# Kernel optimization log

Measured on AMD Instinct MI355X. Metric: run time of the kernel, lower is better.

## Reference

```python
import jax, jax.numpy as jnp
import numpy as np

B, S, D = 2, 2048, 1024
KQ_EMB, V_EMB, H = 1024, 1024, 16
KQ_HD, V_HD = KQ_EMB // H, V_EMB // H


def setup_inputs() -> dict:
    key = jax.random.key(0)
    ks = jax.random.split(key, 7)
    scale = 1.0 / np.sqrt(D)
    return {
        "q": jax.random.normal(ks[0], (B, S, D), dtype=jnp.float32),
        "k": jax.random.normal(ks[1], (B, S, D), dtype=jnp.float32),
        "v": jax.random.normal(ks[2], (B, S, D), dtype=jnp.float32),
        "Wq": jax.random.normal(ks[3], (D, KQ_EMB), dtype=jnp.float32) * scale,
        "Wk": jax.random.normal(ks[4], (D, KQ_EMB), dtype=jnp.float32) * scale,
        "Wv": jax.random.normal(ks[5], (D, V_EMB), dtype=jnp.float32) * scale,
        "Wo": jax.random.normal(ks[6], (V_EMB, V_EMB), dtype=jnp.float32) * (1.0 / np.sqrt(V_EMB)),
        "masked": 1,
    }


def reference(q, k, v, Wq, Wk, Wv, Wo, masked):
    Bq, Sq, _ = q.shape
    # projections (Linear, no bias)
    Q = (q @ Wq).reshape(Bq, Sq, H, KQ_HD).transpose(0, 2, 1, 3)  # [B,H,S,hd]
    K = (k @ Wk).reshape(Bq, Sq, H, KQ_HD).transpose(0, 2, 1, 3)
    V = (v @ Wv).reshape(Bq, Sq, H, V_HD).transpose(0, 2, 1, 3)
    scores = jnp.einsum("bhqd,bhkd->bhqk", Q, K) * (1.0 / KQ_HD ** 0.5)
    if masked:
        causal = jnp.tril(jnp.ones((Sq, Sq), dtype=bool))  # True = keep
        scores = jnp.where(causal, scores, jnp.float32(-jnp.inf))
    weights = jax.nn.softmax(scores, axis=-1)
    attn_out = jnp.einsum("bhqk,bhkd->bhqd", weights, V)  # [B,H,S,v_hd]
    merged = attn_out.transpose(0, 2, 1, 3).reshape(Bq, Sq, H * V_HD)
    output = merged @ Wo
    return output, attn_out
```

## Files before the change

### kernel.cpp

```cpp
#include <hip/hip_runtime.h>
#include <math.h>

constexpr int CB = 2, CS = 2048, CD = 1024, CH = 16, CHD = 64;
constexpr int CEMB = 1024;

typedef unsigned short ushort_t;
typedef __attribute__((ext_vector_type(8))) short short8;
typedef __attribute__((ext_vector_type(4))) float f32x4;

__device__ __forceinline__ ushort_t f2bf(float x) {
    unsigned int u = __builtin_bit_cast(unsigned int, x);
    u = u + 0x7fffu + ((u >> 16) & 1u);
    return (ushort_t)(u >> 16);
}
__device__ __forceinline__ float bf2f(ushort_t h) {
    unsigned int u = ((unsigned int)h) << 16;
    return __builtin_bit_cast(float, u);
}

__global__ __launch_bounds__(256) void convert_wt(
    const float* __restrict__ W0, const float* __restrict__ W1,
    const float* __restrict__ W2, const float* __restrict__ W3,
    ushort_t* __restrict__ H0, ushort_t* __restrict__ L0,
    ushort_t* __restrict__ H1, ushort_t* __restrict__ L1,
    ushort_t* __restrict__ H2, ushort_t* __restrict__ L2,
    ushort_t* __restrict__ H3, ushort_t* __restrict__ L3) {
    const float* W;
    ushort_t* Hd;
    ushort_t* Ld;
    switch (blockIdx.z) {
        case 0: W = W0; Hd = H0; Ld = L0; break;
        case 1: W = W1; Hd = H1; Ld = L1; break;
        case 2: W = W2; Hd = H2; Ld = L2; break;
        default: W = W3; Hd = H3; Ld = L3; break;
    }
    const int n0 = blockIdx.x * 64, k0 = blockIdx.y * 64;
    __shared__ float Ls[64][65];
    const int t = threadIdx.x;
#pragma unroll
    for (int rep = 0; rep < 4; rep++) {
        const int r = rep * 16 + (t >> 4);
        const int c4 = (t & 15) * 4;
        *(float4*)&Ls[r][c4] = *(const float4*)&W[(size_t)(k0 + r) * CEMB + n0 + c4];
    }
    __syncthreads();
    const int n = t >> 2, kc = (t & 3) * 16;
#pragma unroll
    for (int c = 0; c < 2; c++) {
        union { ushort_t us[8]; uint4 v; } H, L;
#pragma unroll
        for (int j = 0; j < 8; j++) {
            const float x = Ls[kc + c * 8 + j][n];
            const ushort_t h = f2bf(x);
            H.us[j] = h;
            L.us[j] = f2bf(x - bf2f(h));
        }
        const size_t dst = (size_t)(n0 + n) * CEMB + k0 + kc + c * 8;
        *(uint4*)&Hd[dst] = H.v;
        *(uint4*)&Ld[dst] = L.v;
    }
}

constexpr int LP = 72;

template <bool GATHER_A>
__device__ __forceinline__ void gemm_split_body(
    const float* __restrict__ A, const ushort_t* __restrict__ Bhi,
    const ushort_t* __restrict__ Blo, float* __restrict__ Cf,
    ushort_t* __restrict__ C0, ushort_t* __restrict__ C1, float scale,
    int emode, bool full, int row0, int col0, int M, int N, int K) {
    __shared__ char gpool[36864];
    ushort_t* const As_hi = (ushort_t*)gpool;
    ushort_t* const As_lo = As_hi + 128 * 32;
    ushort_t* const Bs_hi = As_lo + 128 * 32;
    ushort_t* const Bs_lo = Bs_hi + 128 * 32;
    const int tid = threadIdx.x;
    const int w = tid >> 6, l = tid & 63, lr = l & 15, lg = l >> 4;
    const int wm = w >> 1, wn = w & 1;

    f32x4 acc[4][4];
#pragma unroll
    for (int i = 0; i < 4; i++)
#pragma unroll
        for (int j = 0; j < 4; j++) acc[i][j] = (f32x4)(0.f);

    const int st_r = tid >> 1;
    const int st_kh = (tid & 1) * 16;

    for (int k0 = 0; k0 < K; k0 += 32) {
        {
            const int gm = row0 + st_r;
            const int gk = k0 + st_kh;
            const float* src;
            if (GATHER_A) {
                const int b_ = gm >> 11, s_ = gm & 2047;
                const int h_ = gk >> 6, d_ = gk & 63;
                src = &A[(((size_t)b_ * CH + h_) * CS + s_) * CHD + d_];
            } else {
                src = &A[(size_t)gm * K + gk];
            }
            float va[16];
#pragma unroll
            for (int r = 0; r < 4; r++)
                *(float4*)&va[r * 4] = *(const float4*)&src[r * 4];
#pragma unroll
            for (int c = 0; c < 2; c++) {
                union { ushort_t us[8]; uint4 v; } H, L;
#pragma unroll
                for (int j = 0; j < 8; j++) {
                    const float x = va[c * 8 + j];
                    const ushort_t h = f2bf(x);
                    H.us[j] = h;
                    L.us[j] = f2bf(x - bf2f(h));
                }
                const int chunk = (st_kh >> 3) + c;
                const int csw = chunk ^ ((st_r >> 1) & 3);
                *(uint4*)&As_hi[st_r * 32 + csw * 8] = H.v;
                if (full) *(uint4*)&As_lo[st_r * 32 + csw * 8] = L.v;
            }
        }
        {
            const size_t base = (size_t)(col0 + st_r) * K + k0 + st_kh;
#pragma unroll
            for (int c = 0; c < 2; c++) {
                const int chunk = (st_kh >> 3) + c;
                const int csw = chunk ^ ((st_r >> 1) & 3);
                *(uint4*)&Bs_hi[st_r * 32 + csw * 8] =
                    *(const uint4*)&Bhi[base + c * 8];
                if (full)
                    *(uint4*)&Bs_lo[st_r * 32 + csw * 8] =
                        *(const uint4*)&Blo[base + c * 8];
            }
        }
        __syncthreads();

        short8 ah[4], al[4], bh[4], bl[4];
#pragma unroll
        for (int i = 0; i < 4; i++) {
            const int r = wm * 64 + i * 16 + lr;
            const int cs = lg ^ ((r >> 1) & 3);
            ah[i] = *(const short8*)&As_hi[r * 32 + cs * 8];
            if (full) al[i] = *(const short8*)&As_lo[r * 32 + cs * 8];
        }
#pragma unroll
        for (int j = 0; j < 4; j++) {
            const int cc = wn * 64 + j * 16 + lr;
            const int cs = lg ^ ((cc >> 1) & 3);
            bh[j] = *(const short8*)&Bs_hi[cc * 32 + cs * 8];
            if (full) bl[j] = *(const short8*)&Bs_lo[cc * 32 + cs * 8];
        }
#pragma unroll
        for (int j = 0; j < 4; j++)
#pragma unroll
            for (int i = 0; i < 4; i++) {
                if (full) {
                    acc[i][j] = __builtin_amdgcn_mfma_f32_16x16x32_bf16(
                        al[i], bh[j], acc[i][j], 0, 0, 0);
                    acc[i][j] = __builtin_amdgcn_mfma_f32_16x16x32_bf16(
                        ah[i], bl[j], acc[i][j], 0, 0, 0);
                }
                acc[i][j] = __builtin_amdgcn_mfma_f32_16x16x32_bf16(
                    ah[i], bh[j], acc[i][j], 0, 0, 0);
            }
        __syncthreads();
    }

    if (emode == 2) {
        ushort_t* const T = (ushort_t*)gpool + w * 64 * LP;
#pragma unroll
        for (int i = 0; i < 4; i++)
#pragma unroll
            for (int j = 0; j < 4; j++) {
                const unsigned int a =
                    (unsigned int)f2bf(acc[i][j][0]) |
                    ((unsigned int)f2bf(acc[i][j][1]) << 16);
                const unsigned int b =
                    (unsigned int)f2bf(acc[i][j][2]) |
                    ((unsigned int)f2bf(acc[i][j][3]) << 16);
                *(uint2*)&T[(j * 16 + lr) * LP + i * 16 + 4 * lg] =
                    make_uint2(a, b);
            }
#pragma unroll
        for (int grp = 0; grp < 8; grp++) {
            const int dl = (l >> 3) + grp * 8;
            const int s8 = (l & 7) * 8;
            const uint4 vv = *(const uint4*)&T[dl * LP + s8];
            const int gm = row0 + wm * 64 + s8;
            const int b_ = gm >> 11, ss = gm & 2047;
            const int dg = col0 + wn * 64 + dl;
            const int h_ = dg >> 6, hd = dg & 63;
            *(uint4*)&C0[(((size_t)b_ * CH + h_) * CHD + hd) * CS + ss] = vv;
        }
        return;
    }

#pragma unroll
    for (int i = 0; i < 4; i++)
#pragma unroll
        for (int j = 0; j < 4; j++) {
            const int cc = col0 + wn * 64 + j * 16 + lr;
#pragma unroll
            for (int r = 0; r < 4; r++) {
                const int cr = row0 + wm * 64 + i * 16 + lg * 4 + r;
                const float vv = acc[i][j][r];
                if (emode == 0) {
                    Cf[(size_t)cr * N + cc] = vv;
                } else {
                    const int b_ = cr >> 11, s_ = cr & 2047;
                    const int h_ = cc >> 6, d_ = cc & 63;
                    const size_t idx =
                        (((size_t)b_ * CH + h_) * CS + s_) * CHD + d_;
                    const float x = vv * scale;
                    const ushort_t hb = f2bf(x);
                    C0[idx] = hb;
                    C1[idx] = f2bf(x - bf2f(hb));
                }
            }
        }
}

__global__ __launch_bounds__(256, 2) void qkv_proj(
    const float* __restrict__ q, const float* __restrict__ k,
    const float* __restrict__ v,
    const ushort_t* __restrict__ hq, const ushort_t* __restrict__ lq,
    const ushort_t* __restrict__ hk, const ushort_t* __restrict__ lk,
    const ushort_t* __restrict__ hv, const ushort_t* __restrict__ lv,
    ushort_t* __restrict__ Qhi, ushort_t* __restrict__ Qlo,
    ushort_t* __restrict__ Khi, ushort_t* __restrict__ Klo,
    ushort_t* __restrict__ Vt) {
    const int id = blockIdx.x;
    const int col = id / 96;
    const int rem = id % 96;
    const int z = rem >> 5;
    const int row = rem & 31;
    const float* A;
    const ushort_t* Bh;
    const ushort_t* Bl;
    ushort_t* C0;
    ushort_t* C1 = nullptr;
    float scale = 1.0f;
    int emode;
    bool full = true;
    if (z == 0) {
        A = q; Bh = hq; Bl = lq; C0 = Qhi; C1 = Qlo; scale = 0.125f; emode = 1;
    } else if (z == 1) {
        A = k; Bh = hk; Bl = lk; C0 = Khi; C1 = Klo; emode = 1;
    } else {
        A = v; Bh = hv; Bl = lv; C0 = Vt; emode = 2; full = false;
    }
    gemm_split_body<false>(A, Bh, Bl, nullptr, C0, C1, scale, emode, full,
                           row * 128, col * 128, CB * CS, CEMB, CD);
}

__global__ __launch_bounds__(256, 2) void out_proj(
    const float* __restrict__ attn, const ushort_t* __restrict__ ho,
    const ushort_t* __restrict__ lo_, float* __restrict__ out) {
    const int id = blockIdx.x;
    const int col = id >> 5;
    const int row = id & 31;
    gemm_split_body<true>(attn, ho, lo_, out, nullptr, nullptr, 1.0f, 0, true,
                          row * 128, col * 128, CB * CS, CEMB, CEMB);
}

constexpr int PB = 136;
constexpr int PF = 68;

__global__ __launch_bounds__(256, 2) void flash_mfma(
    const ushort_t* __restrict__ Qhi, const ushort_t* __restrict__ Qlo,
    const ushort_t* __restrict__ Khi, const ushort_t* __restrict__ Klo,
    const ushort_t* __restrict__ Vt, float* __restrict__ O,
    const int* __restrict__ maskedp) {
    __shared__ ushort_t lds[3 * 64 * LP + 4 * 16 * PB];
    ushort_t* const Ks_hi = lds;
    ushort_t* const Ks_lo = lds + 64 * LP;
    ushort_t* const Vs = lds + 2 * 64 * LP;

    const int tid = threadIdx.x;
    const int w = tid >> 6, l = tid & 63, lr = l & 15, lg = l >> 4;
    ushort_t* const Ps = lds + 3 * 64 * LP + w * 16 * PB;
    float* const T = (float*)Ps;
    const int masked = maskedp[0];

    const int id = blockIdx.x + 16 * blockIdx.y;
    const int sid = (id & 7) * 64 + (id >> 3);
    const int jj = sid & 15;
    const int bh = sid >> 4;
    const int qa = 31 - jj;
    const size_t bhoff = (size_t)bh * CS * CHD;

    const int itersA = masked ? (32 - jj) : 32;
    const int TOT = itersA + (masked ? (jj + 1) : 32);

    short8 qh[2], ql[2];
    auto loadQ = [&](int qt) {
        const int q0 = qt * 64 + w * 16;
#pragma unroll
        for (int ds = 0; ds < 2; ds++) {
            const size_t off =
                bhoff + (size_t)(q0 + lr) * CHD + ds * 32 + lg * 8;
            qh[ds] = *(const short8*)&Qhi[off];
            ql[ds] = *(const short8*)&Qlo[off];
        }
    };

    f32x4 Oacc[4];
    float m_i, l_i;
    auto resetState = [&]() {
        m_i = -INFINITY;
        l_i = 0.f;
#pragma unroll
        for (int df = 0; df < 4; df++) Oacc[df] = (f32x4)(0.f);
    };

    auto writeO = [&](int qt) {
        const int q0 = qt * 64 + w * 16;
        const float inv = 1.0f / l_i;
#pragma unroll
        for (int df = 0; df < 4; df++)
            *(f32x4*)&T[lr * PF + df * 16 + 4 * lg] = Oacc[df] * inv;
#pragma unroll
        for (int grp = 0; grp < 4; grp++) {
            const int qrow = grp * 4 + lg;
            const float4 vv = *(const float4*)&T[qrow * PF + lr * 4];
            *(float4*)&O[bhoff + (size_t)(q0 + qrow) * CHD + lr * 4] = vv;
        }
    };

    loadQ(qa);
    resetState();

    const int st_r = tid >> 2;
    const int st_c = tid & 3;

    uint4 pk_hi[2], pk_lo[2], pv[2];
#pragma unroll
    for (int p = 0; p < 2; p++) {
        const int c = st_c + p * 4;
        const size_t kgl = bhoff + (size_t)st_r * CHD + c * 8;
        pk_hi[p] = *(const uint4*)&Khi[kgl];
        pk_lo[p] = *(const uint4*)&Klo[kgl];
        const size_t vgl = ((size_t)bh * CHD + st_r) * CS + c * 8;
        pv[p] = *(const uint4*)&Vt[vgl];
    }

    for (int it = 0; it < TOT; it++) {
        const bool inB = it >= itersA;
        const int t = inB ? (it - itersA) : it;
        const int qtcur = inB ? jj : qa;

#pragma unroll
        for (int p = 0; p < 2; p++) {
            const int c = st_c + p * 4;
            *(uint4*)&Ks_hi[st_r * LP + c * 8] = pk_hi[p];
            *(uint4*)&Ks_lo[st_r * LP + c * 8] = pk_lo[p];
            *(uint4*)&Vs[st_r * LP + c * 8] = pv[p];
        }
        __syncthreads();

        const int nit = it + 1;
        if (nit < TOT) {
            const int nt = (nit >= itersA) ? (nit - itersA) : nit;
#pragma unroll
            for (int p = 0; p < 2; p++) {
                const int c = st_c + p * 4;
                const size_t kgl =
                    bhoff + (size_t)(nt * 64 + st_r) * CHD + c * 8;
                pk_hi[p] = *(const uint4*)&Khi[kgl];
                pk_lo[p] = *(const uint4*)&Klo[kgl];
                const size_t vgl =
                    ((size_t)bh * CHD + st_r) * CS + nt * 64 + c * 8;
                pv[p] = *(const uint4*)&Vt[vgl];
            }
        }

        f32x4 S[4];
#pragma unroll
        for (int kf = 0; kf < 4; kf++) S[kf] = (f32x4)(0.f);
        __builtin_amdgcn_s_setprio(1);
#pragma unroll
        for (int ds = 0; ds < 2; ds++) {
            short8 kh[4], kl[4];
#pragma unroll
            for (int kf = 0; kf < 4; kf++) {
                const int off = (kf * 16 + lr) * LP + ds * 32 + lg * 8;
                kh[kf] = *(const short8*)&Ks_hi[off];
                kl[kf] = *(const short8*)&Ks_lo[off];
            }
#pragma unroll
            for (int kf = 0; kf < 4; kf++) {
                S[kf] = __builtin_amdgcn_mfma_f32_16x16x32_bf16(
                    kh[kf], ql[ds], S[kf], 0, 0, 0);
                S[kf] = __builtin_amdgcn_mfma_f32_16x16x32_bf16(
                    kl[kf], qh[ds], S[kf], 0, 0, 0);
                S[kf] = __builtin_amdgcn_mfma_f32_16x16x32_bf16(
                    kh[kf], qh[ds], S[kf], 0, 0, 0);
            }
        }
        __builtin_amdgcn_s_setprio(0);

        if (masked && t == qtcur) {
            const int qg = qtcur * 64 + w * 16 + lr;
#pragma unroll
            for (int kf = 0; kf < 4; kf++)
#pragma unroll
                for (int r = 0; r < 4; r++) {
                    const int kg = t * 64 + kf * 16 + 4 * lg + r;
                    if (kg > qg) S[kf][r] = -INFINITY;
                }
        }

        {
            float mt = -INFINITY;
#pragma unroll
            for (int kf = 0; kf < 4; kf++)
#pragma unroll
                for (int r = 0; r < 4; r++) mt = fmaxf(mt, S[kf][r]);
            mt = fmaxf(mt, __shfl_xor(mt, 16));
            mt = fmaxf(mt, __shfl_xor(mt, 32));
            const float mn = fmaxf(m_i, mt);
            const float corr = __expf(m_i - mn);
            float rs = 0.f;
#pragma unroll
            for (int kf = 0; kf < 4; kf++)
#pragma unroll
                for (int r = 0; r < 4; r++) {
                    const float p = __expf(S[kf][r] - mn);
                    S[kf][r] = p;
                    rs += p;
                }
            rs += __shfl_xor(rs, 16);
            rs += __shfl_xor(rs, 32);
            l_i = l_i * corr + rs;
            m_i = mn;
#pragma unroll
            for (int df = 0; df < 4; df++) Oacc[df] *= corr;
        }

#pragma unroll
        for (int kf = 0; kf < 4; kf++) {
            const unsigned int a = (unsigned int)f2bf(S[kf][0]) |
                                   ((unsigned int)f2bf(S[kf][1]) << 16);
            const unsigned int b = (unsigned int)f2bf(S[kf][2]) |
                                   ((unsigned int)f2bf(S[kf][3]) << 16);
            *(uint2*)&Ps[lr * PB + kf * 16 + 4 * lg] = make_uint2(a, b);
        }

        __builtin_amdgcn_s_setprio(1);
#pragma unroll
        for (int ks = 0; ks < 2; ks++) {
            short8 vb[4];
#pragma unroll
            for (int df = 0; df < 4; df++)
                vb[df] = *(const short8*)&Vs[(df * 16 + lr) * LP + ks * 32 +
                                             lg * 8];
            const short8 pb = *(const short8*)&Ps[lr * PB + ks * 32 + lg * 8];
#pragma unroll
            for (int df = 0; df < 4; df++)
                Oacc[df] = __builtin_amdgcn_mfma_f32_16x16x32_bf16(
                    vb[df], pb, Oacc[df], 0, 0, 0);
        }
        __builtin_amdgcn_s_setprio(0);

        if (it == itersA - 1) {
            writeO(qa);
            resetState();
            loadQ(jj);
        }
        __syncthreads();
    }

    writeO(jj);
}

extern "C" void kernel_launch(void* const* d_in, const int* in_sizes, int n_in,
                              void* d_out, int out_size, void* d_ws,
                              size_t ws_size, hipStream_t stream) {
    const float* q  = (const float*)d_in[0];
    const float* k  = (const float*)d_in[1];
    const float* v  = (const float*)d_in[2];
    const float* Wq = (const float*)d_in[3];
    const float* Wk = (const float*)d_in[4];
    const float* Wv = (const float*)d_in[5];
    const float* Wo = (const float*)d_in[6];
    const int* masked = (const int*)d_in[7];

    float* out  = (float*)d_out;
    float* attn = out + (size_t)CB * CS * CEMB;

    const size_t NE = (size_t)CB * CS * CEMB;
    ushort_t* wsb = (ushort_t*)d_ws;
    ushort_t* Qhi = wsb + 0 * NE;
    ushort_t* Qlo = wsb + 1 * NE;
    ushort_t* Khi = wsb + 2 * NE;
    ushort_t* Klo = wsb + 3 * NE;
    ushort_t* Vt  = wsb + 4 * NE;
    ushort_t* wb  = wsb + 5 * NE;
    const size_t WN = (size_t)CEMB * CEMB;
    ushort_t* hq = wb + 0 * WN;  ushort_t* lq = wb + 1 * WN;
    ushort_t* hk = wb + 2 * WN;  ushort_t* lk = wb + 3 * WN;
    ushort_t* hv = wb + 4 * WN;  ushort_t* lv = wb + 5 * WN;
    ushort_t* ho = wb + 6 * WN;  ushort_t* lo_ = wb + 7 * WN;

    dim3 blk(256);

    convert_wt<<<dim3(16, 16, 4), blk, 0, stream>>>(
        Wq, Wk, Wv, Wo, hq, lq, hk, lk, hv, lv, ho, lo_);

    qkv_proj<<<dim3(768), blk, 0, stream>>>(
        q, k, v, hq, lq, hk, lk, hv, lv, Qhi, Qlo, Khi, Klo, Vt);

    flash_mfma<<<dim3(16, CB * CH), blk, 0, stream>>>(
        Qhi, Qlo, Khi, Klo, Vt, attn, masked);

    out_proj<<<dim3(256), blk, 0, stream>>>(attn, ho, lo_, out);
}
```

Measured before the change: 349.3 us.

## Split paired causal q-tiles into separate blocks and XOR-swizzle LDS layout

The flash attention kernel no longer pairs a long and a short causal query tile per block. It now launches one block per q-tile, 1024 blocks in total, with the longest tiles scheduled first and each XCD grouped onto a few heads. The padded LDS rows are replaced with an XOR-swizzled 64-wide layout that avoids bank conflicts while using less shared memory, and occupancy is raised to 3 blocks per CU. This trades the balanced per-block work of the pairing scheme for more parallelism and relies on the hardware scheduler for load balance.

After: 376.9 us. 1.08x slower.

```diff
diff --git a/kernel.cpp b/kernel.cpp
--- a/kernel.cpp
+++ b/kernel.cpp
@@ -262,73 +262,43 @@
                           row * 128, col * 128, CB * CS, CEMB, CEMB);
 }
 
-constexpr int PB = 136;
-constexpr int PF = 68;
-
-__global__ __launch_bounds__(256, 2) void flash_mfma(
+__global__ __launch_bounds__(256, 3) void flash_mfma(
     const ushort_t* __restrict__ Qhi, const ushort_t* __restrict__ Qlo,
     const ushort_t* __restrict__ Khi, const ushort_t* __restrict__ Klo,
     const ushort_t* __restrict__ Vt, float* __restrict__ O,
     const int* __restrict__ maskedp) {
-    __shared__ ushort_t lds[3 * 64 * LP + 4 * 16 * PB];
+    __shared__ ushort_t lds[4 * 64 * 64];
     ushort_t* const Ks_hi = lds;
-    ushort_t* const Ks_lo = lds + 64 * LP;
-    ushort_t* const Vs = lds + 2 * 64 * LP;
+    ushort_t* const Ks_lo = lds + 64 * 64;
+    ushort_t* const Vs = lds + 2 * 64 * 64;
 
     const int tid = threadIdx.x;
     const int w = tid >> 6, l = tid & 63, lr = l & 15, lg = l >> 4;
-    ushort_t* const Ps = lds + 3 * 64 * LP + w * 16 * PB;
-    float* const T = (float*)Ps;
+    ushort_t* const Ps = lds + 3 * 64 * 64 + w * 16 * 64;
     const int masked = maskedp[0];
 
-    const int id = blockIdx.x + 16 * blockIdx.y;
-    const int sid = (id & 7) * 64 + (id >> 3);
-    const int jj = sid & 15;
-    const int bh = sid >> 4;
-    const int qa = 31 - jj;
+    const int id = blockIdx.x;
+    const int xcd = id & 7;
+    const int local = id >> 3;
+    const int bh = xcd * 4 + (local & 3);
+    const int qt = 31 - (local >> 2);
+    const int q0 = qt * 64 + w * 16;
     const size_t bhoff = (size_t)bh * CS * CHD;
 
-    const int itersA = masked ? (32 - jj) : 32;
-    const int TOT = itersA + (masked ? (jj + 1) : 32);
-
     short8 qh[2], ql[2];
-    auto loadQ = [&](int qt) {
-        const int q0 = qt * 64 + w * 16;
-#pragma unroll
-        for (int ds = 0; ds < 2; ds++) {
-            const size_t off =
-                bhoff + (size_t)(q0 + lr) * CHD + ds * 32 + lg * 8;
-            qh[ds] = *(const short8*)&Qhi[off];
-            ql[ds] = *(const short8*)&Qlo[off];
-        }
-    };
+#pragma unroll
+    for (int ds = 0; ds < 2; ds++) {
+        const size_t off = bhoff + (size_t)(q0 + lr) * CHD + ds * 32 + lg * 8;
+        qh[ds] = *(const short8*)&Qhi[off];
+        ql[ds] = *(const short8*)&Qlo[off];
+    }
 
     f32x4 Oacc[4];
-    float m_i, l_i;
-    auto resetState = [&]() {
-        m_i = -INFINITY;
-        l_i = 0.f;
-#pragma unroll
-        for (int df = 0; df < 4; df++) Oacc[df] = (f32x4)(0.f);
-    };
-
-    auto writeO = [&](int qt) {
-        const int q0 = qt * 64 + w * 16;
-        const float inv = 1.0f / l_i;
-#pragma unroll
-        for (int df = 0; df < 4; df++)
-            *(f32x4*)&T[lr * PF + df * 16 + 4 * lg] = Oacc[df] * inv;
-#pragma unroll
-        for (int grp = 0; grp < 4; grp++) {
-            const int qrow = grp * 4 + lg;
-            const float4 vv = *(const float4*)&T[qrow * PF + lr * 4];
-            *(float4*)&O[bhoff + (size_t)(q0 + qrow) * CHD + lr * 4] = vv;
-        }
-    };
-
-    loadQ(qa);
-    resetState();
-
+    float m_i = -INFINITY, l_i = 0.f;
+#pragma unroll
+    for (int df = 0; df < 4; df++) Oacc[df] = (f32x4)(0.f);
+
+    const int tmax = masked ? qt : 31;
     const int st_r = tid >> 2;
     const int st_c = tid & 3;
 
@@ -343,32 +313,27 @@
         pv[p] = *(const uint4*)&Vt[vgl];
     }
 
-    for (int it = 0; it < TOT; it++) {
-        const bool inB = it >= itersA;
-        const int t = inB ? (it - itersA) : it;
-        const int qtcur = inB ? jj : qa;
-
+    for (int t = 0; t <= tmax; t++) {
 #pragma unroll
         for (int p = 0; p < 2; p++) {
             const int c = st_c + p * 4;
-            *(uint4*)&Ks_hi[st_r * LP + c * 8] = pk_hi[p];
-            *(uint4*)&Ks_lo[st_r * LP + c * 8] = pk_lo[p];
-            *(uint4*)&Vs[st_r * LP + c * 8] = pv[p];
+            const int dst = st_r * 64 + (c ^ (st_r & 7)) * 8;
+            *(uint4*)&Ks_hi[dst] = pk_hi[p];
+            *(uint4*)&Ks_lo[dst] = pk_lo[p];
+            *(uint4*)&Vs[dst] = pv[p];
         }
         __syncthreads();
 
-        const int nit = it + 1;
-        if (nit < TOT) {
-            const int nt = (nit >= itersA) ? (nit - itersA) : nit;
+        if (t < tmax) {
 #pragma unroll
             for (int p = 0; p < 2; p++) {
                 const int c = st_c + p * 4;
                 const size_t kgl =
-                    bhoff + (size_t)(nt * 64 + st_r) * CHD + c * 8;
+                    bhoff + (size_t)((t + 1) * 64 + st_r) * CHD + c * 8;
                 pk_hi[p] = *(const uint4*)&Khi[kgl];
                 pk_lo[p] = *(const uint4*)&Klo[kgl];
                 const size_t vgl =
-                    ((size_t)bh * CHD + st_r) * CS + nt * 64 + c * 8;
+                    ((size_t)bh * CHD + st_r) * CS + (t + 1) * 64 + c * 8;
                 pv[p] = *(const uint4*)&Vt[vgl];
             }
         }
@@ -382,7 +347,8 @@
             short8 kh[4], kl[4];
 #pragma unroll
             for (int kf = 0; kf < 4; kf++) {
-                const int off = (kf * 16 + lr) * LP + ds * 32 + lg * 8;
+                const int off =
+                    (kf * 16 + lr) * 64 + (((ds * 4 + lg) ^ (lr & 7)) * 8);
                 kh[kf] = *(const short8*)&Ks_hi[off];
                 kl[kf] = *(const short8*)&Ks_lo[off];
             }
@@ -398,8 +364,8 @@
         }
         __builtin_amdgcn_s_setprio(0);
 
-        if (masked && t == qtcur) {
-            const int qg = qtcur * 64 + w * 16 + lr;
+        if (masked && t == qt) {
+            const int qg = q0 + lr;
 #pragma unroll
             for (int kf = 0; kf < 4; kf++)
 #pragma unroll
@@ -442,7 +408,10 @@
                                    ((unsigned int)f2bf(S[kf][1]) << 16);
             const unsigned int b = (unsigned int)f2bf(S[kf][2]) |
                                    ((unsigned int)f2bf(S[kf][3]) << 16);
-            *(uint2*)&Ps[lr * PB + kf * 16 + 4 * lg] = make_uint2(a, b);
+            const int off = lr * 64 +
+                            (((2 * kf + (lg >> 1)) ^ (lr & 7)) * 8) +
+                            (lg & 1) * 4;
+            *(uint2*)&Ps[off] = make_uint2(a, b);
         }
 
         __builtin_amdgcn_s_setprio(1);
@@ -451,9 +420,11 @@
             short8 vb[4];
 #pragma unroll
             for (int df = 0; df < 4; df++)
-                vb[df] = *(const short8*)&Vs[(df * 16 + lr) * LP + ks * 32 +
-                                             lg * 8];
-            const short8 pb = *(const short8*)&Ps[lr * PB + ks * 32 + lg * 8];
+                vb[df] = *(const short8*)&Vs[(df * 16 + lr) * 64 +
+                                             (((ks * 4 + lg) ^ (lr & 7)) * 8)];
+            const short8 pb = *(const short8*)&Ps[lr * 64 +
+                                                  (((ks * 4 + lg) ^ (lr & 7)) *
+                                                   8)];
 #pragma unroll
             for (int df = 0; df < 4; df++)
                 Oacc[df] = __builtin_amdgcn_mfma_f32_16x16x32_bf16(
@@ -461,15 +432,23 @@
         }
         __builtin_amdgcn_s_setprio(0);
 
-        if (it == itersA - 1) {
-            writeO(qa);
-            resetState();
-            loadQ(jj);
-        }
         __syncthreads();
     }
 
-    writeO(jj);
+    float* const T = (float*)lds + (size_t)w * 16 * 64;
+    const float inv = 1.0f / l_i;
+#pragma unroll
+    for (int df = 0; df < 4; df++) {
+        *(f32x4*)&T[lr * 64 + (((df * 4 + lg) ^ (lr & 7)) * 4)] =
+            Oacc[df] * inv;
+    }
+#pragma unroll
+    for (int grp = 0; grp < 4; grp++) {
+        const int qrow = grp * 4 + lg;
+        const float4 vv =
+            *(const float4*)&T[qrow * 64 + ((lr ^ (qrow & 7)) * 4)];
+        *(float4*)&O[bhoff + (size_t)(q0 + qrow) * CHD + lr * 4] = vv;
+    }
 }
 
 extern "C" void kernel_launch(void* const* d_in, const int* in_sizes, int n_in,
@@ -509,7 +488,7 @@
     qkv_proj<<<dim3(768), blk, 0, stream>>>(
         q, k, v, hq, lq, hk, lk, hv, lv, Qhi, Qlo, Khi, Klo, Vt);
 
-    flash_mfma<<<dim3(16, CB * CH), blk, 0, stream>>>(
+    flash_mfma<<<dim3(1024), blk, 0, stream>>>(
         Qhi, Qlo, Khi, Klo, Vt, attn, masked);
 
     out_proj<<<dim3(256), blk, 0, stream>>>(attn, ho, lo_, out);
```
